# Kernel tuning notes

Measured on AMD Instinct MI355X. Metric: run time of the kernel, lower is better.

## Reference

```python
import jax, jax.numpy as jnp
import numpy as np

DIM = 8192


def setup_inputs() -> dict:
    key = jax.random.key(0)
    k0, k1, k2, k3 = jax.random.split(key, 4)
    # Four trajectory points of the flattened parameter vector.
    x0 = jax.random.normal(k0, (DIM,), dtype=jnp.float32)
    x1 = jax.random.normal(k1, (DIM,), dtype=jnp.float32)
    x2 = jax.random.normal(k2, (DIM,), dtype=jnp.float32)
    x3 = jax.random.normal(k3, (DIM,), dtype=jnp.float32)
    return {"x0": x0, "x1": x1, "x2": x2, "x3": x3}


def reference(x0, x1, x2, x3):
    # Successive differences along the trajectory
    d0 = x1 - x0
    d1 = x2 - x1
    d2 = x3 - x2
    D1 = jnp.stack([d0, d1], axis=1)  # [dim, 2]
    D2 = jnp.stack([d1, d2], axis=1)  # [dim, 2]
    # M = D2 @ pinv(D1): dense [dim, dim] (rank <= 2)
    M = D2 @ jnp.linalg.pinv(D1)
    dim = x0.shape[0]
    B = jnp.eye(dim, dtype=x0.dtype) - M
    z = x1 - M @ x0
    # B is square and generically full rank (I minus rank-2), so
    # lstsq(B, z) == solve(B, z).
    x_star = jnp.linalg.solve(B, z)
    # update = current params (x0) - fixed point estimate
    return x0 - x_star
```

## Files before the change

kernel.cpp:

```cpp
#include <hip/hip_runtime.h>


#define ETF_NT  1024
#define ETF_NW  (ETF_NT / 64)

__global__ __launch_bounds__(ETF_NT) void etf_fused_kernel(
    const float* __restrict__ x0, const float* __restrict__ x1,
    const float* __restrict__ x2, const float* __restrict__ x3,
    float* __restrict__ out) {
  const int t = threadIdx.x;

  const float4* X0 = reinterpret_cast<const float4*>(x0);
  const float4* X1 = reinterpret_cast<const float4*>(x1);
  const float4* X2 = reinterpret_cast<const float4*>(x2);
  const float4* X3 = reinterpret_cast<const float4*>(x3);

  float4 u0 = X0[t], v0 = X0[t + ETF_NT];
  float4 u1 = X1[t], v1 = X1[t + ETF_NT];
  float4 u2 = X2[t], v2 = X2[t + ETF_NT];
  float4 u3 = X3[t], v3 = X3[t + ETF_NT];

  float e0[8] = {u0.x, u0.y, u0.z, u0.w, v0.x, v0.y, v0.z, v0.w};
  float e1[8] = {u1.x, u1.y, u1.z, u1.w, v1.x, v1.y, v1.z, v1.w};
  float e2[8] = {u2.x, u2.y, u2.z, u2.w, v2.x, v2.y, v2.z, v2.w};
  float e3[8] = {u3.x, u3.y, u3.z, u3.w, v3.x, v3.y, v3.z, v3.w};

  double g00 = 0.0, g01 = 0.0, g11 = 0.0, s01 = 0.0, s11 = 0.0;
  double p0 = 0.0, p1 = 0.0, q0 = 0.0, q1 = 0.0;

#pragma unroll
  for (int k = 0; k < 8; ++k) {
    double d0 = (double)(e1[k] - e0[k]);
    double d1 = (double)(e2[k] - e1[k]);
    double d2 = (double)(e3[k] - e2[k]);
    g00 += d0 * d0;
    g01 += d0 * d1;
    g11 += d1 * d1;
    s01 += d0 * d2;
    s11 += d1 * d2;
    p0 += d0 * (double)e0[k];
    p1 += d1 * (double)e0[k];
    q0 += d0 * (double)e1[k];
    q1 += d1 * (double)e1[k];
  }

#pragma unroll
  for (int off = 32; off > 0; off >>= 1) {
    g00 += __shfl_down(g00, off);
    g01 += __shfl_down(g01, off);
    g11 += __shfl_down(g11, off);
    s01 += __shfl_down(s01, off);
    s11 += __shfl_down(s11, off);
    p0 += __shfl_down(p0, off);
    p1 += __shfl_down(p1, off);
    q0 += __shfl_down(q0, off);
    q1 += __shfl_down(q1, off);
  }

  __shared__ double red[ETF_NW][9];
  __shared__ float coef[2];

  const int wave = t >> 6;
  const int lane = t & 63;
  if (lane == 0) {
    red[wave][0] = g00; red[wave][1] = g01; red[wave][2] = g11;
    red[wave][3] = s01; red[wave][4] = s11;
    red[wave][5] = p0;  red[wave][6] = p1;
    red[wave][7] = q0;  red[wave][8] = q1;
  }
  __syncthreads();

  if (t == 0) {
    double G00 = 0, G01 = 0, G11 = 0, S01 = 0, S11 = 0;
    double P0 = 0, P1 = 0, Q0 = 0, Q1 = 0;
#pragma unroll
    for (int w = 0; w < ETF_NW; ++w) {
      G00 += red[w][0]; G01 += red[w][1]; G11 += red[w][2];
      S01 += red[w][3]; S11 += red[w][4];
      P0 += red[w][5];  P1 += red[w][6];
      Q0 += red[w][7];  Q1 += red[w][8];
    }
    const double det = G00 * G11 - G01 * G01;
    const double inv = 1.0 / det;
    const double a0 = (G11 * P0 - G01 * P1) * inv;
    const double a1 = (G00 * P1 - G01 * P0) * inv;
    const double w01 = (G11 * S01 - G01 * S11) * inv;
    const double w11 = (G00 * S11 - G01 * S01) * inv;
    const double r0 = Q0 - (G01 * a0 + S01 * a1);
    const double r1 = Q1 - (G11 * a0 + S11 * a1);
    const double t0 = (G11 * r0 - G01 * r1) * inv;
    const double t1 = (G00 * r1 - G01 * r0) * inv;
    const double detK = (1.0 - w11) - w01;
    const double c0 = ((1.0 - w11) * t0 + w01 * t1) / detK;
    const double c1 = (t0 + t1) / detK;
    coef[0] = (float)(c0 - a0);
    coef[1] = (float)(c1 - a1);
  }
  __syncthreads();

  const float alpha = coef[0];
  const float beta = coef[1];

  float4* O = reinterpret_cast<float4*>(out);
  float4 o;
  o.x = (u0.x - u1.x) - alpha * (u2.x - u1.x) - beta * (u3.x - u2.x);
  o.y = (u0.y - u1.y) - alpha * (u2.y - u1.y) - beta * (u3.y - u2.y);
  o.z = (u0.z - u1.z) - alpha * (u2.z - u1.z) - beta * (u3.z - u2.z);
  o.w = (u0.w - u1.w) - alpha * (u2.w - u1.w) - beta * (u3.w - u2.w);
  O[t] = o;
  o.x = (v0.x - v1.x) - alpha * (v2.x - v1.x) - beta * (v3.x - v2.x);
  o.y = (v0.y - v1.y) - alpha * (v2.y - v1.y) - beta * (v3.y - v2.y);
  o.z = (v0.z - v1.z) - alpha * (v2.z - v1.z) - beta * (v3.z - v2.z);
  o.w = (v0.w - v1.w) - alpha * (v2.w - v1.w) - beta * (v3.w - v2.w);
  O[t + ETF_NT] = o;
}

extern "C" void kernel_launch(void* const* d_in, const int* in_sizes, int n_in,
                              void* d_out, int out_size, void* d_ws, size_t ws_size,
                              hipStream_t stream) {
  const float* x0 = (const float*)d_in[0];
  const float* x1 = (const float*)d_in[1];
  const float* x2 = (const float*)d_in[2];
  const float* x3 = (const float*)d_in[3];
  float* out = (float*)d_out;
  (void)in_sizes; (void)n_in; (void)out_size; (void)d_ws; (void)ws_size;

  etf_fused_kernel<<<1, ETF_NT, 0, stream>>>(x0, x1, x2, x3, out);
}
```

Before: 63.99 us.

## Split fused reduction across 16 cooperative blocks with a grid-wide sync

Replaces the single 1024-thread block with 16 blocks of 128 threads launched cooperatively. Each block reduces its slice of the nine Gram and projection sums, publishes them to workspace with release stores, and after a grid sync every block reads all partials back and recomputes the two coefficients. This spreads the loads over more compute units to cut the single-CU latency, but adds a cooperative launch and a grid barrier, whose overhead is significant for a kernel this small.

```diff
diff --git a/kernel.cpp b/kernel.cpp
--- a/kernel.cpp
+++ b/kernel.cpp
@@ -1,35 +1,41 @@
 #include <hip/hip_runtime.h>
+#include <hip/hip_cooperative_groups.h>
+
+namespace cg = cooperative_groups;
 
 
-#define ETF_NT  1024
-#define ETF_NW  (ETF_NT / 64)
+#define ETF_NB   16
+#define ETF_NT   128
+#define ETF_NWV  (ETF_NT / 64)
 
-__global__ __launch_bounds__(ETF_NT) void etf_fused_kernel(
-    const float* __restrict__ x0, const float* __restrict__ x1,
-    const float* __restrict__ x2, const float* __restrict__ x3,
-    float* __restrict__ out) {
+__global__ __launch_bounds__(ETF_NT) void etf_coop_kernel(
+    const float* __restrict__ x0p, const float* __restrict__ x1p,
+    const float* __restrict__ x2p, const float* __restrict__ x3p,
+    float* __restrict__ out, double* __restrict__ ws) {
   const int t = threadIdx.x;
+  const int b = blockIdx.x;
+  const int g = b * ETF_NT + t;
 
-  const float4* X0 = reinterpret_cast<const float4*>(x0);
-  const float4* X1 = reinterpret_cast<const float4*>(x1);
-  const float4* X2 = reinterpret_cast<const float4*>(x2);
-  const float4* X3 = reinterpret_cast<const float4*>(x3);
+  const float4* X0 = reinterpret_cast<const float4*>(x0p);
+  const float4* X1 = reinterpret_cast<const float4*>(x1p);
+  const float4* X2 = reinterpret_cast<const float4*>(x2p);
+  const float4* X3 = reinterpret_cast<const float4*>(x3p);
 
-  float4 u0 = X0[t], v0 = X0[t + ETF_NT];
-  float4 u1 = X1[t], v1 = X1[t + ETF_NT];
-  float4 u2 = X2[t], v2 = X2[t + ETF_NT];
-  float4 u3 = X3[t], v3 = X3[t + ETF_NT];
+  float4 u0 = X0[g];
+  float4 u1 = X1[g];
+  float4 u2 = X2[g];
+  float4 u3 = X3[g];
 
-  float e0[8] = {u0.x, u0.y, u0.z, u0.w, v0.x, v0.y, v0.z, v0.w};
-  float e1[8] = {u1.x, u1.y, u1.z, u1.w, v1.x, v1.y, v1.z, v1.w};
-  float e2[8] = {u2.x, u2.y, u2.z, u2.w, v2.x, v2.y, v2.z, v2.w};
-  float e3[8] = {u3.x, u3.y, u3.z, u3.w, v3.x, v3.y, v3.z, v3.w};
+  float e0[4] = {u0.x, u0.y, u0.z, u0.w};
+  float e1[4] = {u1.x, u1.y, u1.z, u1.w};
+  float e2[4] = {u2.x, u2.y, u2.z, u2.w};
+  float e3[4] = {u3.x, u3.y, u3.z, u3.w};
 
   double g00 = 0.0, g01 = 0.0, g11 = 0.0, s01 = 0.0, s11 = 0.0;
   double p0 = 0.0, p1 = 0.0, q0 = 0.0, q1 = 0.0;
 
 #pragma unroll
-  for (int k = 0; k < 8; ++k) {
+  for (int k = 0; k < 4; ++k) {
     double d0 = (double)(e1[k] - e0[k]);
     double d1 = (double)(e2[k] - e1[k]);
     double d2 = (double)(e3[k] - e2[k]);
@@ -57,7 +63,8 @@
     q1 += __shfl_down(q1, off);
   }
 
-  __shared__ double red[ETF_NW][9];
+  __shared__ double red[ETF_NWV][9];
+  __shared__ double comp[9];
   __shared__ float coef[2];
 
   const int wave = t >> 6;
@@ -71,15 +78,30 @@
   __syncthreads();
 
   if (t == 0) {
-    double G00 = 0, G01 = 0, G11 = 0, S01 = 0, S11 = 0;
-    double P0 = 0, P1 = 0, Q0 = 0, Q1 = 0;
 #pragma unroll
-    for (int w = 0; w < ETF_NW; ++w) {
-      G00 += red[w][0]; G01 += red[w][1]; G11 += red[w][2];
-      S01 += red[w][3]; S11 += red[w][4];
-      P0 += red[w][5];  P1 += red[w][6];
-      Q0 += red[w][7];  Q1 += red[w][8];
+    for (int j = 0; j < 9; ++j) {
+      double s = red[0][j] + red[1][j];
+      __hip_atomic_store(&ws[b * 9 + j], s, __ATOMIC_RELEASE,
+                         __HIP_MEMORY_SCOPE_AGENT);
     }
+  }
+
+  cg::this_grid().sync();
+
+  if (t < 9) {
+    double s = 0.0;
+#pragma unroll
+    for (int i = 0; i < ETF_NB; ++i)
+      s += __hip_atomic_load(&ws[i * 9 + t], __ATOMIC_ACQUIRE,
+                             __HIP_MEMORY_SCOPE_AGENT);
+    comp[t] = s;
+  }
+  __syncthreads();
+
+  if (t == 0) {
+    const double G00 = comp[0], G01 = comp[1], G11 = comp[2];
+    const double S01 = comp[3], S11 = comp[4];
+    const double P0 = comp[5], P1 = comp[6], Q0 = comp[7], Q1 = comp[8];
     const double det = G00 * G11 - G01 * G01;
     const double inv = 1.0 / det;
     const double a0 = (G11 * P0 - G01 * P1) * inv;
@@ -107,12 +129,7 @@
   o.y = (u0.y - u1.y) - alpha * (u2.y - u1.y) - beta * (u3.y - u2.y);
   o.z = (u0.z - u1.z) - alpha * (u2.z - u1.z) - beta * (u3.z - u2.z);
   o.w = (u0.w - u1.w) - alpha * (u2.w - u1.w) - beta * (u3.w - u2.w);
-  O[t] = o;
-  o.x = (v0.x - v1.x) - alpha * (v2.x - v1.x) - beta * (v3.x - v2.x);
-  o.y = (v0.y - v1.y) - alpha * (v2.y - v1.y) - beta * (v3.y - v2.y);
-  o.z = (v0.z - v1.z) - alpha * (v2.z - v1.z) - beta * (v3.z - v2.z);
-  o.w = (v0.w - v1.w) - alpha * (v2.w - v1.w) - beta * (v3.w - v2.w);
-  O[t + ETF_NT] = o;
+  O[g] = o;
 }
 
 extern "C" void kernel_launch(void* const* d_in, const int* in_sizes, int n_in,
@@ -123,7 +140,11 @@
   const float* x2 = (const float*)d_in[2];
   const float* x3 = (const float*)d_in[3];
   float* out = (float*)d_out;
-  (void)in_sizes; (void)n_in; (void)out_size; (void)d_ws; (void)ws_size;
+  double* ws = (double*)d_ws;
+  (void)in_sizes; (void)n_in; (void)out_size; (void)ws_size;
 
-  etf_fused_kernel<<<1, ETF_NT, 0, stream>>>(x0, x1, x2, x3, out);
+  void* args[] = {(void*)&x0, (void*)&x1, (void*)&x2, (void*)&x3,
+                  (void*)&out, (void*)&ws};
+  hipLaunchCooperativeKernel((const void*)etf_coop_kernel, dim3(ETF_NB),
+                             dim3(ETF_NT), args, 0, stream);
 }
```

Result: slower. 90.64 us (+41.6%).
